# Kernel tuning notes

Measured on AMD Instinct MI355X. Metric: run time of the kernel, lower is better.

The kernel has to match this reference:

```python
import jax, jax.numpy as jnp
import numpy as np

B = 64          # batch
IN_CH = 128     # in_channels
OUT_CH = 128    # out_channels
MODES = 64      # modes1
N = 4096        # spatial length (power of two -> pad branches in original are no-ops)


def _fht1d(x):
    """Faithful vectorized version of the recursive fht1d.

    x: (M, n) with n a power of two. Same DIT recursion as the torch code:
    X = [E + cas*O, E - cas*O], cas(theta) = cos(theta) + sin(theta).
    Even/odd halves are stacked along the leading axis so the recursion is
    traced only log2(n) times (fully vectorized at each level).
    """
    n = x.shape[-1]
    if n == 1:
        return x
    sub = _fht1d(jnp.concatenate([x[:, 0::2], x[:, 1::2]], axis=0))  # (2M, n/2)
    e, o = jnp.split(sub, 2, axis=0)
    k = jnp.arange(n // 2, dtype=x.dtype)
    theta = (2.0 * jnp.pi / n) * k
    cas = jnp.cos(theta) + jnp.sin(theta)
    t = cas * o
    return jnp.concatenate([e + t, e - t], axis=-1)


def dht_last(x):
    """DHT along the last dim of x (B, C, N); N is a power of two."""
    shp = x.shape
    return _fht1d(x.reshape(-1, shp[-1])).reshape(shp)


def compl_mul1d(x1, x2):
    # x1: (b, i, m), x2: (i, o, m); Hartley-domain "complex" multiply.
    neg = lambda a: jnp.roll(jnp.flip(a, axis=-1), 1, axis=-1)  # H(-k)
    x1n = neg(x1)
    x2n = neg(x2)
    return 0.5 * (
        jnp.einsum('bix,iox->box', x1, x2)
        - jnp.einsum('bix,iox->box', x1n, x2n)
        + jnp.einsum('bix,iox->box', x1, x2n)
        + jnp.einsum('bix,iox->box', x1n, x2)
    )


def setup_inputs() -> dict:
    key = jax.random.key(0)
    kx, kw = jax.random.split(key)
    x = jax.random.normal(kx, (B, IN_CH, N), dtype=jnp.float32)
    scale = 1.0 / (IN_CH * OUT_CH)
    weights1 = scale * jax.random.uniform(kw, (IN_CH, OUT_CH, MODES), dtype=jnp.float32)
    return {"x": x, "weights1": weights1}


def reference(x, weights1):
    n = x.shape[-1]
    modes = weights1.shape[-1]
    x_ht = dht_last(x)                                  # (B, IN_CH, N)
    mixed = compl_mul1d(x_ht[:, :, :modes], weights1)   # (B, OUT_CH, modes)
    out_ht = jnp.zeros((x.shape[0], weights1.shape[1], n), dtype=x.dtype)
    out_ht = out_ht.at[:, :, :modes].set(mixed)
    # idht = dht / N
    return dht_last(out_ht) / n
```

## Files before the change

kernel.cpp:

```cpp
#include <hip/hip_runtime.h>
#include <math.h>

#define PI2F 6.28318530717958647692f

__host__ __device__ constexpr int br6(int p) {
    return ((p & 1) << 5) | ((p & 2) << 3) | ((p & 4) << 1) |
           ((p & 8) >> 1) | ((p & 16) >> 3) | ((p & 32) >> 5);
}
__host__ __device__ constexpr int brN(int v, int bits) {
    int r = 0;
    for (int i = 0; i < bits; ++i) r |= ((v >> i) & 1) << (bits - 1 - i);
    return r;
}

__device__ static constexpr float CAS8T[4] = {1.f, 1.41421356f, 1.f, 0.f};
__device__ static constexpr float CAS16T[8] = {
    1.f, 1.30656296f, 1.41421356f, 1.30656296f, 1.f, 0.54119610f, 0.f, -0.54119610f};
__device__ static constexpr float CAS32T[16] = {
    1.f, 1.17587560f, 1.30656296f, 1.38703985f, 1.41421356f, 1.38703985f,
    1.30656296f, 1.17587560f, 1.f, 0.78569496f, 0.54119610f, 0.27589938f,
    0.f, -0.27589938f, -0.54119610f, -0.78569496f};
__device__ static constexpr float CAS64T[32] = {
    1.f, 1.09320187f, 1.17587560f, 1.24722502f, 1.30656296f, 1.35331800f,
    1.38703985f, 1.40740373f, 1.41421356f, 1.40740373f, 1.38703985f,
    1.35331800f, 1.30656296f, 1.24722502f, 1.17587560f, 1.09320187f,
    1.f, 0.89716759f, 0.78569496f, 0.66665566f, 0.54119610f, 0.41052452f,
    0.27589938f, 0.13861717f, 0.f, -0.13861717f, -0.27589938f, -0.41052452f,
    -0.54119610f, -0.66665566f, -0.78569496f, -0.89716759f};

__global__ __launch_bounds__(256) void wtrans_cast(const float* __restrict__ w,
                                                   float* __restrict__ wp,
                                                   float* __restrict__ wm,
                                                   float* __restrict__ casT) {
    const int tid = threadIdx.x;
    if (blockIdx.x == 128) {
        if (blockIdx.y != 0) return;
#pragma unroll
        for (int base = 0; base < 4096; base += 256) {
            const int idx = base + tid;
            if (idx < 4032) {
                const int j = idx >> 6, r = idx & 63;
                int l, u;
                if (j == 0) { l = 5; u = 0; }
                else if (j < 3) { l = 4; u = j - 1; }
                else if (j < 7) { l = 3; u = j - 3; }
                else if (j < 15) { l = 2; u = j - 7; }
                else if (j < 31) { l = 1; u = j - 15; }
                else { l = 0; u = j - 31; }
                float s, c;
                sincosf(PI2F * (float)(r + 64 * u) / (float)(4096 >> l), &s, &c);
                casT[j * 64 + r] = c + s;
            }
        }
        return;
    }
    __shared__ float W[64 * 65];
    const int i = blockIdx.x;
    const int oh = blockIdx.y;
    const float* src = w + (size_t)i * 8192 + oh * 4096;
#pragma unroll
    for (int it = 0; it < 4; ++it) {
        const int k = it * 1024 + tid * 4;
        const float4 v = *(const float4*)(src + k);
        const int ol = k >> 6;
        const int ml = k & 63;
        W[ol * 65 + ml + 0] = v.x;
        W[ol * 65 + ml + 1] = v.y;
        W[ol * 65 + ml + 2] = v.z;
        W[ol * 65 + ml + 3] = v.w;
    }
    __syncthreads();
    const int mh = tid >> 6;
    const int ol = tid & 63;
    const int o = oh * 64 + ol;
#pragma unroll
    for (int ml = 0; ml < 16; ++ml) {
        const int m = mh * 16 + ml;
        const int mp = (64 - m) & 63;
        const float a = W[ol * 65 + m];
        const float b = W[ol * 65 + mp];
        wp[((size_t)m * 128 + i) * 128 + o] = 0.5f * (a + b);
        wm[((size_t)m * 128 + i) * 128 + o] = 0.5f * (a - b);
    }
}

__global__ __launch_bounds__(64) void fht_fwd(const float* __restrict__ x,
                                              float* __restrict__ xh_t) {
    __shared__ float Y[64 * 65];
    const int lane = threadIdx.x;

    float a6[6];
#pragma unroll
    for (int l = 0; l < 6; ++l) {
        float s, c;
        sincosf(PI2F * (float)lane / (float)(4096 >> l), &s, &c);
        a6[l] = c + s;
    }
    float G[64];
    G[0] = 1.0f;
#pragma unroll
    for (int c = 1; c < 64; ++c) G[c] = G[c & (c - 1)] * a6[__builtin_ctz(c)];

    const int row0 = blockIdx.x * 2;
#pragma unroll 1
    for (int rr = 0; rr < 2; ++rr) {
        const int row = row0 + rr;
        const float* xr = x + (size_t)row * 4096 + lane;
        float v[64];
#pragma unroll
        for (int p = 0; p < 64; ++p) v[p] = xr[64 * br6(p)];

#pragma unroll
        for (int b = 0; b < 64; b += 2) {
            float t0 = v[b], t1 = v[b + 1];
            v[b] = t0 + t1; v[b + 1] = t0 - t1;
        }
#pragma unroll
        for (int b = 0; b < 64; b += 4)
#pragma unroll
            for (int k = 0; k < 2; ++k) {
                float t0 = v[b + k], t1 = v[b + k + 2];
                v[b + k] = t0 + t1; v[b + k + 2] = t0 - t1;
            }
#pragma unroll
        for (int b = 0; b < 64; b += 8)
#pragma unroll
            for (int k = 0; k < 4; ++k) {
                float w = CAS8T[k];
                float t0 = v[b + k], t1 = v[b + k + 4];
                v[b + k] = fmaf(w, t1, t0); v[b + k + 4] = fmaf(-w, t1, t0);
            }
#pragma unroll
        for (int b = 0; b < 64; b += 16)
#pragma unroll
            for (int k = 0; k < 8; ++k) {
                float w = CAS16T[k];
                float t0 = v[b + k], t1 = v[b + k + 8];
                v[b + k] = fmaf(w, t1, t0); v[b + k + 8] = fmaf(-w, t1, t0);
            }
#pragma unroll
        for (int b = 0; b < 64; b += 32)
#pragma unroll
            for (int k = 0; k < 16; ++k) {
                float w = CAS32T[k];
                float t0 = v[b + k], t1 = v[b + k + 16];
                v[b + k] = fmaf(w, t1, t0); v[b + k + 16] = fmaf(-w, t1, t0);
            }
#pragma unroll
        for (int k = 0; k < 32; ++k) {
            float w = CAS64T[k];
            float t0 = v[k], t1 = v[k + 32];
            v[k] = fmaf(w, t1, t0); v[k + 32] = fmaf(-w, t1, t0);
        }

#pragma unroll
        for (int m = 0; m < 64; ++m) Y[lane * 65 + m] = v[m];
        __syncthreads();
        float acc = 0.0f;
#pragma unroll
        for (int c = 0; c < 64; ++c) acc = fmaf(G[c], Y[c * 65 + lane], acc);
        __syncthreads();
        xh_t[(size_t)lane * 8192 + row] = acc;
    }
}

__global__ __launch_bounds__(256) void passB(const float* __restrict__ xh_t,
                                             const float* __restrict__ wp,
                                             const float* __restrict__ wm,
                                             float* __restrict__ mixed_t) {
    __shared__ float Us[16][136];
    __shared__ float Uns[16][136];
    const int tid = threadIdx.x;
    const int m = blockIdx.y;
    const int bt = blockIdx.x;
    const int mp = (64 - m) & 63;
#pragma unroll
    for (int it = 0; it < 2; ++it) {
        const int slot = tid + it * 256;
        const int b = slot >> 5;
        const int i0 = (slot & 31) * 4;
        const float4 vu = *(const float4*)(xh_t + (size_t)m  * 8192 + bt * 2048 + slot * 4);
        const float4 vn = *(const float4*)(xh_t + (size_t)mp * 8192 + bt * 2048 + slot * 4);
        *(float4*)&Us[b][i0] = vu;
        *(float4*)&Uns[b][i0] = vn;
    }
    __syncthreads();
    const int b = tid >> 4;
    const int o0 = (tid & 15) * 8;
    float acc[8];
#pragma unroll
    for (int j = 0; j < 8; ++j) acc[j] = 0.0f;
#pragma unroll 2
    for (int i = 0; i < 128; ++i) {
        float p[8], q[8];
        *(float4*)&p[0] = *(const float4*)(wp + ((size_t)m * 128 + i) * 128 + o0);
        *(float4*)&p[4] = *(const float4*)(wp + ((size_t)m * 128 + i) * 128 + o0 + 4);
        *(float4*)&q[0] = *(const float4*)(wm + ((size_t)m * 128 + i) * 128 + o0);
        *(float4*)&q[4] = *(const float4*)(wm + ((size_t)m * 128 + i) * 128 + o0 + 4);
        const float u = Us[b][i];
        const float un = Uns[b][i];
#pragma unroll
        for (int j = 0; j < 8; ++j) acc[j] += u * p[j] + un * q[j];
    }
    float* dst = mixed_t + (size_t)m * 8192 + (bt * 16 + b) * 128 + o0;
    *(float4*)dst = make_float4(acc[0], acc[1], acc[2], acc[3]);
    *(float4*)(dst + 4) = make_float4(acc[4], acc[5], acc[6], acc[7]);
}

__global__ __launch_bounds__(64) void fht_inv(const float* __restrict__ mixed_t,
                                              const float* __restrict__ casT,
                                              float* __restrict__ out) {
    __shared__ __align__(16) float S[64];
    const int lane = threadIdx.x;
    float K[63];
#pragma unroll
    for (int j = 0; j < 63; ++j) K[j] = casT[j * 64 + lane];

    const int row0 = blockIdx.x * 4;
#pragma unroll 1
    for (int rr = 0; rr < 4; ++rr) {
        const int row = row0 + rr;
        const float mv = mixed_t[(size_t)lane * 8192 + row] * (1.0f / 4096.0f);
        __syncthreads();
        S[lane] = mv;
        __syncthreads();
        float e[64];
#pragma unroll
        for (int m4 = 0; m4 < 16; ++m4) {
            const float4 q = *(const float4*)&S[4 * m4];
            e[4 * m4 + 0] = q.x; e[4 * m4 + 1] = q.y;
            e[4 * m4 + 2] = q.z; e[4 * m4 + 3] = q.w;
        }
#pragma unroll
        for (int mp = 0; mp < 32; ++mp) {
            float w = K[0];
            float t0 = e[mp], t1 = e[mp + 32];
            e[mp] = fmaf(w, t1, t0); e[mp + 32] = fmaf(-w, t1, t0);
        }
#pragma unroll
        for (int hi = 0; hi < 2; ++hi)
#pragma unroll
            for (int mp = 0; mp < 16; ++mp) {
                float w = K[1 + brN(hi, 1)];
                int i0 = hi * 32 + mp;
                float t0 = e[i0], t1 = e[i0 + 16];
                e[i0] = fmaf(w, t1, t0); e[i0 + 16] = fmaf(-w, t1, t0);
            }
#pragma unroll
        for (int hi = 0; hi < 4; ++hi)
#pragma unroll
            for (int mp = 0; mp < 8; ++mp) {
                float w = K[3 + brN(hi, 2)];
                int i0 = hi * 16 + mp;
                float t0 = e[i0], t1 = e[i0 + 8];
                e[i0] = fmaf(w, t1, t0); e[i0 + 8] = fmaf(-w, t1, t0);
            }
#pragma unroll
        for (int hi = 0; hi < 8; ++hi)
#pragma unroll
            for (int mp = 0; mp < 4; ++mp) {
                float w = K[7 + brN(hi, 3)];
                int i0 = hi * 8 + mp;
                float t0 = e[i0], t1 = e[i0 + 4];
                e[i0] = fmaf(w, t1, t0); e[i0 + 4] = fmaf(-w, t1, t0);
            }
#pragma unroll
        for (int hi = 0; hi < 16; ++hi)
#pragma unroll
            for (int mp = 0; mp < 2; ++mp) {
                float w = K[15 + brN(hi, 4)];
                int i0 = hi * 4 + mp;
                float t0 = e[i0], t1 = e[i0 + 2];
                e[i0] = fmaf(w, t1, t0); e[i0 + 2] = fmaf(-w, t1, t0);
            }
#pragma unroll
        for (int hi = 0; hi < 32; ++hi) {
            float w = K[31 + brN(hi, 5)];
            int i0 = hi * 2;
            float t0 = e[i0], t1 = e[i0 + 1];
            e[i0] = fmaf(w, t1, t0); e[i0 + 1] = fmaf(-w, t1, t0);
        }
        float* outr = out + (size_t)row * 4096 + lane;
#pragma unroll
        for (int t = 0; t < 64; ++t) outr[64 * t] = e[br6(t)];
    }
}

extern "C" void kernel_launch(void* const* d_in, const int* in_sizes, int n_in,
                              void* d_out, int out_size, void* d_ws, size_t ws_size,
                              hipStream_t stream) {
    const float* x = (const float*)d_in[0];
    const float* w = (const float*)d_in[1];
    float* out = (float*)d_out;
    float* wsf = (float*)d_ws;

    float* casT    = wsf + 512;
    float* xh_t    = wsf + 8192;
    float* wp      = wsf + 532480;
    float* wm      = wsf + 1581056;
    float* mixed_t = wsf + 2629632;

    wtrans_cast<<<dim3(129, 2), dim3(256), 0, stream>>>(w, wp, wm, casT);
    fht_fwd<<<dim3(4096), dim3(64), 0, stream>>>(x, xh_t);
    passB<<<dim3(4, 64), dim3(256), 0, stream>>>(xh_t, wp, wm, mixed_t);
    fht_inv<<<dim3(2048), dim3(64), 0, stream>>>(mixed_t, casT, out);
}
```

Before: 274.4 us.

## Stage FHT row loads and stores through LDS with float4 accesses, retile passB

```diff
diff --git a/kernel.cpp b/kernel.cpp
--- a/kernel.cpp
+++ b/kernel.cpp
@@ -102,13 +102,20 @@
     for (int c = 1; c < 64; ++c) G[c] = G[c & (c - 1)] * a6[__builtin_ctz(c)];
 
     const int row0 = blockIdx.x * 2;
+    float accs[2];
 #pragma unroll 1
     for (int rr = 0; rr < 2; ++rr) {
-        const int row = row0 + rr;
-        const float* xr = x + (size_t)row * 4096 + lane;
+        const float* xr = x + (size_t)(row0 + rr) * 4096;
+#pragma unroll
+        for (int j = 0; j < 16; ++j) {
+            const float4 v4 = *(const float4*)(xr + (j * 64 + lane) * 4);
+            *(float4*)&Y[(j * 64 + lane) * 4] = v4;
+        }
+        __syncthreads();
         float v[64];
 #pragma unroll
-        for (int p = 0; p < 64; ++p) v[p] = xr[64 * br6(p)];
+        for (int p = 0; p < 64; ++p) v[p] = Y[64 * br6(p) + lane];
+        __syncthreads();
 
 #pragma unroll
         for (int b = 0; b < 64; b += 2) {
@@ -160,56 +167,53 @@
 #pragma unroll
         for (int c = 0; c < 64; ++c) acc = fmaf(G[c], Y[c * 65 + lane], acc);
         __syncthreads();
-        xh_t[(size_t)lane * 8192 + row] = acc;
-    }
+        accs[rr] = acc;
+    }
+    *(float2*)(xh_t + (size_t)lane * 8192 + row0) = make_float2(accs[0], accs[1]);
 }
 
 __global__ __launch_bounds__(256) void passB(const float* __restrict__ xh_t,
                                              const float* __restrict__ wp,
                                              const float* __restrict__ wm,
                                              float* __restrict__ mixed_t) {
-    __shared__ float Us[16][136];
-    __shared__ float Uns[16][136];
+    __shared__ float Us[8][132];
+    __shared__ float Uns[8][132];
     const int tid = threadIdx.x;
     const int m = blockIdx.y;
     const int bt = blockIdx.x;
     const int mp = (64 - m) & 63;
-#pragma unroll
-    for (int it = 0; it < 2; ++it) {
-        const int slot = tid + it * 256;
-        const int b = slot >> 5;
-        const int i0 = (slot & 31) * 4;
-        const float4 vu = *(const float4*)(xh_t + (size_t)m  * 8192 + bt * 2048 + slot * 4);
-        const float4 vn = *(const float4*)(xh_t + (size_t)mp * 8192 + bt * 2048 + slot * 4);
-        *(float4*)&Us[b][i0] = vu;
-        *(float4*)&Uns[b][i0] = vn;
+    {
+        const int bl = tid >> 5;
+        const int i0 = (tid & 31) * 4;
+        const float4 vu = *(const float4*)(xh_t + (size_t)m  * 8192 + bt * 1024 + tid * 4);
+        const float4 vn = *(const float4*)(xh_t + (size_t)mp * 8192 + bt * 1024 + tid * 4);
+        *(float4*)&Us[bl][i0] = vu;
+        *(float4*)&Uns[bl][i0] = vn;
     }
     __syncthreads();
-    const int b = tid >> 4;
-    const int o0 = (tid & 15) * 8;
-    float acc[8];
-#pragma unroll
-    for (int j = 0; j < 8; ++j) acc[j] = 0.0f;
-#pragma unroll 2
+    const int b = tid >> 5;
+    const int o0 = (tid & 31) * 4;
+    float acc[4];
+#pragma unroll
+    for (int j = 0; j < 4; ++j) acc[j] = 0.0f;
+#pragma unroll 4
     for (int i = 0; i < 128; ++i) {
-        float p[8], q[8];
+        float p[4], q[4];
         *(float4*)&p[0] = *(const float4*)(wp + ((size_t)m * 128 + i) * 128 + o0);
-        *(float4*)&p[4] = *(const float4*)(wp + ((size_t)m * 128 + i) * 128 + o0 + 4);
         *(float4*)&q[0] = *(const float4*)(wm + ((size_t)m * 128 + i) * 128 + o0);
-        *(float4*)&q[4] = *(const float4*)(wm + ((size_t)m * 128 + i) * 128 + o0 + 4);
         const float u = Us[b][i];
         const float un = Uns[b][i];
 #pragma unroll
-        for (int j = 0; j < 8; ++j) acc[j] += u * p[j] + un * q[j];
-    }
-    float* dst = mixed_t + (size_t)m * 8192 + (bt * 16 + b) * 128 + o0;
+        for (int j = 0; j < 4; ++j) acc[j] += u * p[j] + un * q[j];
+    }
+    float* dst = mixed_t + (size_t)m * 8192 + (bt * 8 + b) * 128 + o0;
     *(float4*)dst = make_float4(acc[0], acc[1], acc[2], acc[3]);
-    *(float4*)(dst + 4) = make_float4(acc[4], acc[5], acc[6], acc[7]);
 }
 
 __global__ __launch_bounds__(64) void fht_inv(const float* __restrict__ mixed_t,
                                               const float* __restrict__ casT,
                                               float* __restrict__ out) {
+    __shared__ float OS[4096];
     __shared__ __align__(16) float S[64];
     const int lane = threadIdx.x;
     float K[63];
@@ -217,12 +221,16 @@
     for (int j = 0; j < 63; ++j) K[j] = casT[j * 64 + lane];
 
     const int row0 = blockIdx.x * 4;
+    float4 mv4 = *(const float4*)(mixed_t + (size_t)lane * 8192 + row0);
+    mv4.x *= (1.0f / 4096.0f); mv4.y *= (1.0f / 4096.0f);
+    mv4.z *= (1.0f / 4096.0f); mv4.w *= (1.0f / 4096.0f);
+    float mvs[4] = {mv4.x, mv4.y, mv4.z, mv4.w};
+
 #pragma unroll 1
     for (int rr = 0; rr < 4; ++rr) {
         const int row = row0 + rr;
-        const float mv = mixed_t[(size_t)lane * 8192 + row] * (1.0f / 4096.0f);
-        __syncthreads();
-        S[lane] = mv;
+        __syncthreads();
+        S[lane] = mvs[rr];
         __syncthreads();
         float e[64];
 #pragma unroll
@@ -280,9 +288,14 @@
             float t0 = e[i0], t1 = e[i0 + 1];
             e[i0] = fmaf(w, t1, t0); e[i0 + 1] = fmaf(-w, t1, t0);
         }
-        float* outr = out + (size_t)row * 4096 + lane;
-#pragma unroll
-        for (int t = 0; t < 64; ++t) outr[64 * t] = e[br6(t)];
+#pragma unroll
+        for (int t = 0; t < 64; ++t) OS[64 * t + lane] = e[br6(t)];
+        __syncthreads();
+        float* outr = out + (size_t)row * 4096;
+#pragma unroll
+        for (int j = 0; j < 16; ++j) {
+            *(float4*)(outr + (j * 64 + lane) * 4) = *(const float4*)&OS[(j * 64 + lane) * 4];
+        }
     }
 }
 
@@ -302,6 +315,6 @@
 
     wtrans_cast<<<dim3(129, 2), dim3(256), 0, stream>>>(w, wp, wm, casT);
     fht_fwd<<<dim3(4096), dim3(64), 0, stream>>>(x, xh_t);
-    passB<<<dim3(4, 64), dim3(256), 0, stream>>>(xh_t, wp, wm, mixed_t);
+    passB<<<dim3(8, 64), dim3(256), 0, stream>>>(xh_t, wp, wm, mixed_t);
     fht_inv<<<dim3(2048), dim3(64), 0, stream>>>(mixed_t, casT, out);
 }
```

Result: faster. 268.1 us (-2.3%).
